# Kernel optimization log

Measured on AMD Instinct MI355X. Metric: run time of the kernel, lower is better.

## Reference

```python
import jax, jax.numpy as jnp
import numpy as np
import math

PI = math.pi

def setup_inputs() -> dict:
    key = jax.random.key(0)
    ks = jax.random.split(key, 12)
    B, L, D, K = 2, 2048, 256, 32
    s = 0.02
    return {
        "x":   jax.random.normal(ks[0], (B, L, D), dtype=jnp.float32),
        "kw1": jax.random.normal(ks[1], (D, D), dtype=jnp.float32) * s,
        "kb1": jnp.zeros((D,), dtype=jnp.float32),
        "kw2": jax.random.normal(ks[2], (K, D), dtype=jnp.float32) * s,
        "kb2": jnp.zeros((K,), dtype=jnp.float32),
        "qw1": jax.random.normal(ks[3], (D, D), dtype=jnp.float32) * s,
        "qb1": jnp.zeros((D,), dtype=jnp.float32),
        "qw2": jax.random.normal(ks[4], (K, D), dtype=jnp.float32) * s,
        "qb2": jnp.zeros((K,), dtype=jnp.float32),
        "vw":  jax.random.normal(ks[5], (D, D), dtype=jnp.float32) * s,
        "vb":  jnp.zeros((D,), dtype=jnp.float32),
    }

def _encode_phase(x, w1, b1, w2, b2):
    # Sequential(Linear, Tanh, Linear) followed by outer tanh * pi in forward
    h = jnp.tanh(jnp.einsum('bld,ed->ble', x, w1) + b1)
    return jnp.tanh(jnp.einsum('bld,kd->blk', h, w2) + b2) * PI

def reference(x, kw1, kb1, kw2, kb2, qw1, qb1, qw2, qb2, vw, vb):
    B, L, D = x.shape
    key_phase = _encode_phase(x, kw1, kb1, kw2, kb2)    # [B,L,K]
    query_phase = _encode_phase(x, qw1, qb1, qw2, qb2)  # [B,L,K]
    K = key_phase.shape[-1]
    value = jnp.einsum('bld,ed->ble', x, vw) + vb       # [B,L,D]

    cos_k = jnp.cos(key_phase)[..., None]               # [B,L,K,1]
    sin_k = jnp.sin(key_phase)[..., None]
    v_exp = value[:, :, None, :]                        # [B,L,1,D]
    mem_real = jnp.cumsum(cos_k * v_exp, axis=1)        # [B,L,K,D]
    mem_imag = jnp.cumsum(sin_k * v_exp, axis=1)

    cos_q = jnp.cos(query_phase)[..., None]
    sin_q = jnp.sin(query_phase)[..., None]
    retrieved = jnp.sum(mem_real * cos_q + mem_imag * sin_q, axis=2)  # [B,L,D]

    positions = jnp.arange(1, L + 1, dtype=x.dtype)
    norm = jnp.sqrt(positions * K)[None, :, None]
    return retrieved / norm
```

## Files before the change

kernel.cpp:

```cpp
#include <hip/hip_runtime.h>
#include <hip/hip_bf16.h>
#include <math.h>

typedef float v4f   __attribute__((ext_vector_type(4)));
typedef float f32x4 __attribute__((ext_vector_type(4)));
typedef short s16x8 __attribute__((ext_vector_type(8)));
typedef __hip_bfloat16 bf16;

#define PI_F 3.14159265358979323846f


__device__ inline unsigned short f2bf(float f) {
    unsigned int b = __float_as_uint(f);
    unsigned int r = (b + 0x7FFFu + ((b >> 16) & 1u)) >> 16;
    return (unsigned short)r;
}
__device__ inline float bf2f(unsigned short u) {
    return __uint_as_float(((unsigned int)u) << 16);
}
__device__ inline void cvt8(const float* __restrict__ src, unsigned short* dst) {
    v4f a = *(const v4f*)src, b = *(const v4f*)(src + 4);
    ushort4 u0, u1;
    u0.x = f2bf(a[0]); u0.y = f2bf(a[1]); u0.z = f2bf(a[2]); u0.w = f2bf(a[3]);
    u1.x = f2bf(b[0]); u1.y = f2bf(b[1]); u1.z = f2bf(b[2]); u1.w = f2bf(b[3]);
    *(ushort4*)dst = u0; *(ushort4*)(dst + 4) = u1;
}

__global__ __launch_bounds__(256) void k_cvtw(
    const float* __restrict__ kw1, const float* __restrict__ qw1,
    const float* __restrict__ vw,  const float* __restrict__ kw2,
    const float* __restrict__ qw2, bf16* __restrict__ Wb, bf16* __restrict__ W2b)
{
    int i8 = blockIdx.x * 256 + threadIdx.x;
    int r = i8 >> 5, c8 = (i8 & 31) * 8;
    const float* src;
    unsigned short* dst;
    if (r < 768) {
        src = (r < 256) ? kw1 + (size_t)r * 256
            : (r < 512) ? qw1 + (size_t)(r - 256) * 256
                        : vw  + (size_t)(r - 512) * 256;
        dst = (unsigned short*)Wb + (size_t)r * 256;
    } else {
        int r2 = r - 768;
        src = (r2 < 32) ? kw2 + (size_t)r2 * 256 : qw2 + (size_t)(r2 - 32) * 256;
        dst = (unsigned short*)W2b + (size_t)r2 * 256;
    }
    cvt8(src + c8, dst + c8);
}

__global__ __launch_bounds__(512) void k_fused(
    const float* __restrict__ X,   const bf16* __restrict__ Wb,
    const float* __restrict__ kb1, const float* __restrict__ qb1,
    const float* __restrict__ vb,  const bf16* __restrict__ W2b,
    const float* __restrict__ kb2, const float* __restrict__ qb2,
    float* __restrict__ KP, float* __restrict__ QP,
    bf16* __restrict__ Vb, bf16* __restrict__ SRg, bf16* __restrict__ SIg)
{
    __shared__ __align__(16) unsigned char smem[50688];
    unsigned short* Abf = (unsigned short*)smem;
    unsigned short* Hkq = (unsigned short*)(smem + 8448);
    unsigned short* Vt  = (unsigned short*)(smem + 25088);
    unsigned short* CKc = (unsigned short*)(smem + 45568);
    unsigned short* CKs = (unsigned short*)(smem + 48128);
    const int tid = threadIdx.x, bid = blockIdx.x;
    const int lane = tid & 63, wid = tid >> 6;
    const int lrow = lane & 15, lk8 = (lane >> 4) * 8, t0 = (lane >> 4) * 4;
    const int bb = bid >> 7, hc = bid & 127;
    const int row0 = bb * 2048 + hc * 16;

    {
        int r = tid >> 5, c8 = (tid & 31) * 8;
        cvt8(X + (size_t)(row0 + r) * 256 + c8, &Abf[r * 264 + c8]);
    }
    {
        s16x8 z = {};
        { int r = tid >> 1, h = tid & 1; *(s16x8*)&Vt[r * 40 + 16 + h * 8] = z; }
        if (tid < 64)       { int r = tid >> 1, h = tid & 1;
                              *(s16x8*)&CKc[r * 40 + 16 + h * 8] = z; }
        else if (tid < 128) { int r = (tid - 64) >> 1, h = tid & 1;
                              *(s16x8*)&CKs[r * 40 + 16 + h * 8] = z; }
    }
    __syncthreads();

    const int nb = wid * 96;
    const unsigned short* Wu = (const unsigned short*)Wb;
    f32x4 acc[6] = {};
    for (int k0 = 0; k0 < 256; k0 += 32) {
        s16x8 a = *(const s16x8*)&Abf[lrow * 264 + k0 + lk8];
        #pragma unroll
        for (int nf = 0; nf < 6; ++nf) {
            s16x8 b = *(const s16x8*)(Wu + (size_t)(nb + nf * 16 + lrow) * 256 + k0 + lk8);
            acc[nf] = __builtin_amdgcn_mfma_f32_16x16x32_bf16(a, b, acc[nf], 0, 0, 0);
        }
    }
    #pragma unroll
    for (int nf = 0; nf < 6; ++nf) {
        int n = nb + nf * 16 + lrow;
        float bias = (n < 256) ? kb1[n] : (n < 512) ? qb1[n - 256] : vb[n - 512];
        if (n < 512) {
            #pragma unroll
            for (int r = 0; r < 4; ++r)
                Hkq[(t0 + r) * 520 + n] = f2bf(tanhf(acc[nf][r] + bias));
        } else {
            int d = n - 512;
            ushort4 u;
            u.x = f2bf(acc[nf][0] + bias); u.y = f2bf(acc[nf][1] + bias);
            u.z = f2bf(acc[nf][2] + bias); u.w = f2bf(acc[nf][3] + bias);
            *(ushort4*)&Vt[d * 40 + t0] = u;
            unsigned short* Vg = (unsigned short*)Vb + (size_t)(row0 + t0) * 256 + d;
            Vg[0] = u.x; Vg[256] = u.y; Vg[512] = u.z; Vg[768] = u.w;
        }
    }
    __syncthreads();

    if (wid < 4) {
        const int which = wid >> 1, nf = wid & 1;
        const unsigned short* W2u = (const unsigned short*)W2b
            + (size_t)(which * 32 + nf * 16 + lrow) * 256;
        f32x4 u = {};
        for (int k0 = 0; k0 < 256; k0 += 32) {
            s16x8 a = *(const s16x8*)&Hkq[lrow * 520 + which * 256 + k0 + lk8];
            s16x8 b = *(const s16x8*)(W2u + k0 + lk8);
            u = __builtin_amdgcn_mfma_f32_16x16x32_bf16(a, b, u, 0, 0, 0);
        }
        const int outk = nf * 16 + lrow;
        const float bias = (which ? qb2 : kb2)[outk];
        float* dst = which ? QP : KP;
        float cs[4], sn[4];
        #pragma unroll
        for (int r = 0; r < 4; ++r) {
            float ph = tanhf(u[r] + bias) * PI_F;
            __sincosf(ph, &sn[r], &cs[r]);
            int row = row0 + t0 + r;
            dst[(size_t)row * 64 + outk]      = cs[r];
            dst[(size_t)row * 64 + 32 + outk] = sn[r];
        }
        if (which == 0) {
            ushort4 uc, us;
            uc.x = f2bf(cs[0]); uc.y = f2bf(cs[1]); uc.z = f2bf(cs[2]); uc.w = f2bf(cs[3]);
            us.x = f2bf(sn[0]); us.y = f2bf(sn[1]); us.z = f2bf(sn[2]); us.w = f2bf(sn[3]);
            *(ushort4*)&CKc[outk * 40 + t0] = uc;
            *(ushort4*)&CKs[outk * 40 + t0] = us;
        }
    }
    __syncthreads();

    {
        f32x4 zz = {};
        s16x8 ac0 = *(const s16x8*)&CKc[lrow * 40 + lk8];
        s16x8 ac1 = *(const s16x8*)&CKc[(16 + lrow) * 40 + lk8];
        s16x8 as0 = *(const s16x8*)&CKs[lrow * 40 + lk8];
        s16x8 as1 = *(const s16x8*)&CKs[(16 + lrow) * 40 + lk8];
        unsigned short* SRu = (unsigned short*)SRg;
        unsigned short* SIu = (unsigned short*)SIg;
        #pragma unroll
        for (int nf = 0; nf < 2; ++nf) {
            int dcol = wid * 32 + nf * 16 + lrow;
            s16x8 bv = *(const s16x8*)&Vt[dcol * 40 + lk8];
            f32x4 r0 = __builtin_amdgcn_mfma_f32_16x16x32_bf16(ac0, bv, zz, 0, 0, 0);
            f32x4 r1 = __builtin_amdgcn_mfma_f32_16x16x32_bf16(ac1, bv, zz, 0, 0, 0);
            f32x4 i0 = __builtin_amdgcn_mfma_f32_16x16x32_bf16(as0, bv, zz, 0, 0, 0);
            f32x4 i1 = __builtin_amdgcn_mfma_f32_16x16x32_bf16(as1, bv, zz, 0, 0, 0);
            size_t base = (((size_t)(bb * 128 + hc)) * 32) * 256 + dcol;
            #pragma unroll
            for (int r = 0; r < 4; ++r) {
                int ka = t0 + r, kb_ = 16 + t0 + r;
                SRu[base + (size_t)ka  * 256] = f2bf(r0[r]);
                SRu[base + (size_t)kb_ * 256] = f2bf(r1[r]);
                SIu[base + (size_t)ka  * 256] = f2bf(i0[r]);
                SIu[base + (size_t)kb_ * 256] = f2bf(i1[r]);
            }
        }
    }
}

__global__ __launch_bounds__(512) void k_scan(
    const bf16* __restrict__ SRh, const bf16* __restrict__ SIh,
    bf16* __restrict__ PFR, bf16* __restrict__ PFI)
{
    int gid = blockIdx.x * 512 + threadIdx.x;
    int e2 = gid & 4095, seg = (gid >> 12) & 7, ri = (gid >> 15) & 1, b = gid >> 16;
    const unsigned short* S = (const unsigned short*)(ri ? SIh : SRh);
    unsigned short* PF = (unsigned short*)(ri ? PFI : PFR);
    const size_t col = (size_t)e2 * 2;
    const size_t hbase = (size_t)(b * 128) * 8192 + col;
    float r0 = 0.f, r1 = 0.f;
    for (int hp = 0; hp < seg * 16; ++hp) {
        ushort2 u = *(const ushort2*)(S + hbase + (size_t)hp * 8192);
        r0 += bf2f(u.x); r1 += bf2f(u.y);
    }
    #pragma unroll
    for (int j = 0; j < 8; ++j) {
        int c = seg * 8 + j;
        ushort2 w; w.x = f2bf(r0); w.y = f2bf(r1);
        *(ushort2*)(PF + (size_t)(b * 64 + c) * 8192 + col) = w;
        ushort2 u0 = *(const ushort2*)(S + hbase + (size_t)(2 * c)     * 8192);
        ushort2 u1 = *(const ushort2*)(S + hbase + (size_t)(2 * c + 1) * 8192);
        r0 += bf2f(u0.x) + bf2f(u1.x);
        r1 += bf2f(u0.y) + bf2f(u1.y);
    }
}

__global__ __launch_bounds__(512) void k_attnout(
    const float* __restrict__ KP, const float* __restrict__ QP,
    const bf16* __restrict__ Vb,
    const bf16* __restrict__ PFR, const bf16* __restrict__ PFI,
    float* __restrict__ out)
{
    __shared__ float sm[18560];
    float* QPc = sm;
    float* KPc = sm + 2176;
    float* Sl  = sm + 4352;
    const int tid = threadIdx.x, bid = blockIdx.x;
    const int group = tid >> 8, t256 = tid & 255;
    float* grp  = sm + 5504 + group * 6528;
    float* vall = grp;
    float* PRl  = grp + 2176;
    float* PIl  = grp + 4352;
    const int b = bid >> 7, c = (bid >> 1) & 63, dhh = bid & 1;
    const int dh = dhh * 2 + group;
    const int row0 = b * 2048 + c * 32;

    #pragma unroll
    for (int it = 0; it < 2; ++it) {
        int idx = t256 + it * 256, t = idx >> 4, j4 = idx & 15;
        *(v4f*)&QPc[t * 68 + j4 * 4] = *(const v4f*)(QP + (size_t)(row0 + t) * 64 + j4 * 4);
        *(v4f*)&KPc[t * 68 + j4 * 4] = *(const v4f*)(KP + (size_t)(row0 + t) * 64 + j4 * 4);
    }
    {
        int t = t256 >> 3, e8 = (t256 & 7) * 8;
        s16x8 u = *(const s16x8*)((const unsigned short*)Vb
                                  + (size_t)(row0 + t) * 256 + dh * 64 + e8);
        #pragma unroll
        for (int j = 0; j < 8; ++j) vall[t * 68 + e8 + j] = bf2f((unsigned short)u[j]);
    }
    {
        int k = t256 >> 3, dg = t256 & 7;
        size_t pb = ((size_t)(b * 64 + c)) * 8192 + k * 256 + dh * 64 + dg * 8;
        s16x8 ur = *(const s16x8*)((const unsigned short*)PFR + pb);
        s16x8 ui = *(const s16x8*)((const unsigned short*)PFI + pb);
        #pragma unroll
        for (int j = 0; j < 8; ++j) {
            PRl[k * 68 + dg * 8 + j] = bf2f((unsigned short)ur[j]);
            PIl[k * 68 + dg * 8 + j] = bf2f((unsigned short)ui[j]);
        }
    }
    __syncthreads();
    {
        const int sl = t256 >> 3, tq = t256 & 7;
        float s4[4] = {0.f, 0.f, 0.f, 0.f};
        for (int j4 = 0; j4 < 16; ++j4) {
            v4f q4 = *(const v4f*)&QPc[sl * 68 + j4 * 4];
            #pragma unroll
            for (int i = 0; i < 4; ++i) {
                v4f k4 = *(const v4f*)&KPc[(tq * 4 + i) * 68 + j4 * 4];
                s4[i] += q4[0]*k4[0] + q4[1]*k4[1] + q4[2]*k4[2] + q4[3]*k4[3];
            }
        }
        #pragma unroll
        for (int i = 0; i < 4; ++i) {
            int t = tq * 4 + i;
            Sl[sl * 36 + t] = (t <= sl) ? s4[i] : 0.f;
        }
    }
    __syncthreads();
    const int l = t256 & 31, dq = t256 >> 5;
    const int d0 = dq * 8;
    float acc[8] = {};
    for (int k = 0; k < 32; ++k) {
        float qc = QPc[l * 68 + k], qs = QPc[l * 68 + 32 + k];
        #pragma unroll
        for (int j4 = 0; j4 < 2; ++j4) {
            v4f pr = *(const v4f*)&PRl[k * 68 + d0 + j4 * 4];
            v4f pi = *(const v4f*)&PIl[k * 68 + d0 + j4 * 4];
            #pragma unroll
            for (int x = 0; x < 4; ++x)
                acc[j4 * 4 + x] += qc * pr[x] + qs * pi[x];
        }
    }
    for (int t = 0; t < 32; ++t) {
        float s = Sl[l * 36 + t];
        #pragma unroll
        for (int j4 = 0; j4 < 2; ++j4) {
            v4f v4_ = *(const v4f*)&vall[t * 68 + d0 + j4 * 4];
            #pragma unroll
            for (int x = 0; x < 4; ++x)
                acc[j4 * 4 + x] = fmaf(s, v4_[x], acc[j4 * 4 + x]);
        }
    }
    const int gl = c * 32 + l;
    const float inv = rsqrtf((float)((gl + 1) * 32));
    const size_t ob = ((size_t)(b * 2048 + gl)) * 256 + dh * 64 + d0;
    #pragma unroll
    for (int j4 = 0; j4 < 2; ++j4) {
        v4f v;
        #pragma unroll
        for (int x = 0; x < 4; ++x) v[x] = acc[j4 * 4 + x] * inv;
        *(v4f*)(out + ob + j4 * 4) = v;
    }
}

extern "C" void kernel_launch(void* const* d_in, const int* in_sizes, int n_in,
                              void* d_out, int out_size, void* d_ws, size_t ws_size,
                              hipStream_t stream)
{
    const float* x   = (const float*)d_in[0];
    const float* kw1 = (const float*)d_in[1];
    const float* kb1 = (const float*)d_in[2];
    const float* kw2 = (const float*)d_in[3];
    const float* kb2 = (const float*)d_in[4];
    const float* qw1 = (const float*)d_in[5];
    const float* qb1 = (const float*)d_in[6];
    const float* qw2 = (const float*)d_in[7];
    const float* qb2 = (const float*)d_in[8];
    const float* vw  = (const float*)d_in[9];
    const float* vb  = (const float*)d_in[10];
    float* out = (float*)d_out;

    char* ws = (char*)d_ws;
    float* KP  = (float*)ws; ws += (size_t)4096 * 64 * 4;
    float* QP  = (float*)ws; ws += (size_t)4096 * 64 * 4;
    bf16*  Wb  = (bf16*)ws;  ws += (size_t)768 * 256 * 2;
    bf16*  W2b = (bf16*)ws;  ws += (size_t)64 * 256 * 2;
    bf16*  Vb  = (bf16*)ws;  ws += (size_t)4096 * 256 * 2;
    bf16*  SRh = (bf16*)ws;  ws += (size_t)2 * 128 * 32 * 256 * 2;
    bf16*  SIh = (bf16*)ws;  ws += (size_t)2 * 128 * 32 * 256 * 2;
    bf16*  PFR = (bf16*)ws;  ws += (size_t)2 * 64 * 32 * 256 * 2;
    bf16*  PFI = (bf16*)ws;  ws += (size_t)2 * 64 * 32 * 256 * 2;

    k_cvtw   <<<104, 256, 0, stream>>>(kw1, qw1, vw, kw2, qw2, Wb, W2b);
    k_fused  <<<256, 512, 0, stream>>>(x, Wb, kb1, qb1, vb, W2b, kb2, qb2,
                                       KP, QP, Vb, SRh, SIh);
    k_scan   <<<256, 512, 0, stream>>>(SRh, SIh, PFR, PFI);
    k_attnout<<<256, 512, 0, stream>>>(KP, QP, Vb, PFR, PFI, out);
}
```

Before: 62.43 us.

## Merge four kernels into one persistent kernel with software grid barriers

Replaces the weight-conversion, fused projection, scan and output kernels with a single 256-block kernel. The stages are separated by a hand-written grid barrier built on per-block flags and a release word in workspace, which is zeroed by a memset before each launch. This is meant to remove the launch gaps and tail effects between the four kernels. In exchange it adds barrier polling cost and a memset, and it depends on all 256 blocks being resident at once (512 threads, about 74 KB LDS each), or the barrier deadlocks.

```diff
diff --git a/kernel.cpp b/kernel.cpp
--- a/kernel.cpp
+++ b/kernel.cpp
@@ -26,277 +26,310 @@
     *(ushort4*)dst = u0; *(ushort4*)(dst + 4) = u1;
 }
 
-__global__ __launch_bounds__(256) void k_cvtw(
-    const float* __restrict__ kw1, const float* __restrict__ qw1,
-    const float* __restrict__ vw,  const float* __restrict__ kw2,
-    const float* __restrict__ qw2, bf16* __restrict__ Wb, bf16* __restrict__ W2b)
+__device__ inline void gridbar(int* flags, int* go, int epoch) {
+    __syncthreads();
+    const int tid = threadIdx.x, bid = blockIdx.x;
+    if (tid == 0) {
+        __threadfence();
+        __hip_atomic_store(&flags[bid], epoch, __ATOMIC_RELAXED,
+                           __HIP_MEMORY_SCOPE_AGENT);
+    }
+    if (bid == 0 && tid < 64) {
+        for (;;) {
+            int ok = 1;
+            #pragma unroll
+            for (int j = 0; j < 4; ++j)
+                ok &= (__hip_atomic_load(&flags[tid + 64 * j], __ATOMIC_RELAXED,
+                                         __HIP_MEMORY_SCOPE_AGENT) >= epoch);
+            if (__all(ok)) break;
+            __builtin_amdgcn_s_sleep(1);
+        }
+        if (tid == 0)
+            __hip_atomic_store(go, epoch, __ATOMIC_RELAXED,
+                               __HIP_MEMORY_SCOPE_AGENT);
+    }
+    if (tid == 0) {
+        while (__hip_atomic_load(go, __ATOMIC_RELAXED,
+                                 __HIP_MEMORY_SCOPE_AGENT) < epoch)
+            __builtin_amdgcn_s_sleep(2);
+        __threadfence();
+    }
+    __syncthreads();
+}
+
+__global__ __launch_bounds__(512) void k_mega(
+    const float* __restrict__ X,
+    const float* __restrict__ kw1, const float* __restrict__ kb1,
+    const float* __restrict__ kw2, const float* __restrict__ kb2,
+    const float* __restrict__ qw1, const float* __restrict__ qb1,
+    const float* __restrict__ qw2, const float* __restrict__ qb2,
+    const float* __restrict__ vw,  const float* __restrict__ vb,
+    float* __restrict__ KP, float* __restrict__ QP,
+    bf16* __restrict__ Wb, bf16* __restrict__ W2b, bf16* __restrict__ Vb,
+    bf16* __restrict__ SRg, bf16* __restrict__ SIg,
+    bf16* __restrict__ PFR, bf16* __restrict__ PFI,
+    float* __restrict__ out, int* __restrict__ bar)
 {
-    int i8 = blockIdx.x * 256 + threadIdx.x;
-    int r = i8 >> 5, c8 = (i8 & 31) * 8;
-    const float* src;
-    unsigned short* dst;
-    if (r < 768) {
-        src = (r < 256) ? kw1 + (size_t)r * 256
-            : (r < 512) ? qw1 + (size_t)(r - 256) * 256
-                        : vw  + (size_t)(r - 512) * 256;
-        dst = (unsigned short*)Wb + (size_t)r * 256;
-    } else {
-        int r2 = r - 768;
-        src = (r2 < 32) ? kw2 + (size_t)r2 * 256 : qw2 + (size_t)(r2 - 32) * 256;
-        dst = (unsigned short*)W2b + (size_t)r2 * 256;
-    }
-    cvt8(src + c8, dst + c8);
-}
-
-__global__ __launch_bounds__(512) void k_fused(
-    const float* __restrict__ X,   const bf16* __restrict__ Wb,
-    const float* __restrict__ kb1, const float* __restrict__ qb1,
-    const float* __restrict__ vb,  const bf16* __restrict__ W2b,
-    const float* __restrict__ kb2, const float* __restrict__ qb2,
-    float* __restrict__ KP, float* __restrict__ QP,
-    bf16* __restrict__ Vb, bf16* __restrict__ SRg, bf16* __restrict__ SIg)
-{
-    __shared__ __align__(16) unsigned char smem[50688];
-    unsigned short* Abf = (unsigned short*)smem;
-    unsigned short* Hkq = (unsigned short*)(smem + 8448);
-    unsigned short* Vt  = (unsigned short*)(smem + 25088);
-    unsigned short* CKc = (unsigned short*)(smem + 45568);
-    unsigned short* CKs = (unsigned short*)(smem + 48128);
+    __shared__ __align__(16) unsigned char smem[74240];
     const int tid = threadIdx.x, bid = blockIdx.x;
-    const int lane = tid & 63, wid = tid >> 6;
-    const int lrow = lane & 15, lk8 = (lane >> 4) * 8, t0 = (lane >> 4) * 4;
-    const int bb = bid >> 7, hc = bid & 127;
-    const int row0 = bb * 2048 + hc * 16;
+    int* flags = bar;
+    int* go    = bar + 320;
 
     {
-        int r = tid >> 5, c8 = (tid & 31) * 8;
-        cvt8(X + (size_t)(row0 + r) * 256 + c8, &Abf[r * 264 + c8]);
-    }
+        int gid = bid * 512 + tid;
+        if (gid < 26624) {
+            int r = gid >> 5, c8 = (gid & 31) * 8;
+            const float* src; unsigned short* dst;
+            if (r < 768) {
+                src = (r < 256) ? kw1 + (size_t)r * 256
+                    : (r < 512) ? qw1 + (size_t)(r - 256) * 256
+                                : vw  + (size_t)(r - 512) * 256;
+                dst = (unsigned short*)Wb + (size_t)r * 256;
+            } else {
+                int r2 = r - 768;
+                src = (r2 < 32) ? kw2 + (size_t)r2 * 256
+                                : qw2 + (size_t)(r2 - 32) * 256;
+                dst = (unsigned short*)W2b + (size_t)r2 * 256;
+            }
+            cvt8(src + c8, dst + c8);
+        }
+    }
+    gridbar(flags, go, 1);
+
     {
-        s16x8 z = {};
-        { int r = tid >> 1, h = tid & 1; *(s16x8*)&Vt[r * 40 + 16 + h * 8] = z; }
-        if (tid < 64)       { int r = tid >> 1, h = tid & 1;
-                              *(s16x8*)&CKc[r * 40 + 16 + h * 8] = z; }
-        else if (tid < 128) { int r = (tid - 64) >> 1, h = tid & 1;
-                              *(s16x8*)&CKs[r * 40 + 16 + h * 8] = z; }
-    }
-    __syncthreads();
-
-    const int nb = wid * 96;
-    const unsigned short* Wu = (const unsigned short*)Wb;
-    f32x4 acc[6] = {};
-    for (int k0 = 0; k0 < 256; k0 += 32) {
-        s16x8 a = *(const s16x8*)&Abf[lrow * 264 + k0 + lk8];
+        unsigned short* Abf = (unsigned short*)smem;
+        unsigned short* Hkq = (unsigned short*)(smem + 8448);
+        unsigned short* Vt  = (unsigned short*)(smem + 25088);
+        unsigned short* CKc = (unsigned short*)(smem + 45568);
+        unsigned short* CKs = (unsigned short*)(smem + 48128);
+        const int lane = tid & 63, wid = tid >> 6;
+        const int lrow = lane & 15, lk8 = (lane >> 4) * 8, t0 = (lane >> 4) * 4;
+        const int bb = bid >> 7, hc = bid & 127;
+        const int row0 = bb * 2048 + hc * 16;
+
+        {
+            int r = tid >> 5, c8 = (tid & 31) * 8;
+            cvt8(X + (size_t)(row0 + r) * 256 + c8, &Abf[r * 264 + c8]);
+        }
+        {
+            s16x8 z = {};
+            { int r = tid >> 1, h = tid & 1; *(s16x8*)&Vt[r * 40 + 16 + h * 8] = z; }
+            if (tid < 64)       { int r = tid >> 1, h = tid & 1;
+                                  *(s16x8*)&CKc[r * 40 + 16 + h * 8] = z; }
+            else if (tid < 128) { int r = (tid - 64) >> 1, h = tid & 1;
+                                  *(s16x8*)&CKs[r * 40 + 16 + h * 8] = z; }
+        }
+        __syncthreads();
+
+        const int nb = wid * 96;
+        const unsigned short* Wu = (const unsigned short*)Wb;
+        f32x4 acc[6] = {};
+        for (int k0 = 0; k0 < 256; k0 += 32) {
+            s16x8 a = *(const s16x8*)&Abf[lrow * 264 + k0 + lk8];
+            #pragma unroll
+            for (int nf = 0; nf < 6; ++nf) {
+                s16x8 b = *(const s16x8*)(Wu + (size_t)(nb + nf * 16 + lrow) * 256 + k0 + lk8);
+                acc[nf] = __builtin_amdgcn_mfma_f32_16x16x32_bf16(a, b, acc[nf], 0, 0, 0);
+            }
+        }
         #pragma unroll
         for (int nf = 0; nf < 6; ++nf) {
-            s16x8 b = *(const s16x8*)(Wu + (size_t)(nb + nf * 16 + lrow) * 256 + k0 + lk8);
-            acc[nf] = __builtin_amdgcn_mfma_f32_16x16x32_bf16(a, b, acc[nf], 0, 0, 0);
-        }
-    }
-    #pragma unroll
-    for (int nf = 0; nf < 6; ++nf) {
-        int n = nb + nf * 16 + lrow;
-        float bias = (n < 256) ? kb1[n] : (n < 512) ? qb1[n - 256] : vb[n - 512];
-        if (n < 512) {
-            #pragma unroll
-            for (int r = 0; r < 4; ++r)
-                Hkq[(t0 + r) * 520 + n] = f2bf(tanhf(acc[nf][r] + bias));
-        } else {
-            int d = n - 512;
-            ushort4 u;
-            u.x = f2bf(acc[nf][0] + bias); u.y = f2bf(acc[nf][1] + bias);
-            u.z = f2bf(acc[nf][2] + bias); u.w = f2bf(acc[nf][3] + bias);
-            *(ushort4*)&Vt[d * 40 + t0] = u;
-            unsigned short* Vg = (unsigned short*)Vb + (size_t)(row0 + t0) * 256 + d;
-            Vg[0] = u.x; Vg[256] = u.y; Vg[512] = u.z; Vg[768] = u.w;
-        }
-    }
-    __syncthreads();
-
-    if (wid < 4) {
-        const int which = wid >> 1, nf = wid & 1;
-        const unsigned short* W2u = (const unsigned short*)W2b
-            + (size_t)(which * 32 + nf * 16 + lrow) * 256;
-        f32x4 u = {};
-        for (int k0 = 0; k0 < 256; k0 += 32) {
-            s16x8 a = *(const s16x8*)&Hkq[lrow * 520 + which * 256 + k0 + lk8];
-            s16x8 b = *(const s16x8*)(W2u + k0 + lk8);
-            u = __builtin_amdgcn_mfma_f32_16x16x32_bf16(a, b, u, 0, 0, 0);
-        }
-        const int outk = nf * 16 + lrow;
-        const float bias = (which ? qb2 : kb2)[outk];
-        float* dst = which ? QP : KP;
-        float cs[4], sn[4];
-        #pragma unroll
-        for (int r = 0; r < 4; ++r) {
-            float ph = tanhf(u[r] + bias) * PI_F;
-            __sincosf(ph, &sn[r], &cs[r]);
-            int row = row0 + t0 + r;
-            dst[(size_t)row * 64 + outk]      = cs[r];
-            dst[(size_t)row * 64 + 32 + outk] = sn[r];
-        }
-        if (which == 0) {
-            ushort4 uc, us;
-            uc.x = f2bf(cs[0]); uc.y = f2bf(cs[1]); uc.z = f2bf(cs[2]); uc.w = f2bf(cs[3]);
-            us.x = f2bf(sn[0]); us.y = f2bf(sn[1]); us.z = f2bf(sn[2]); us.w = f2bf(sn[3]);
-            *(ushort4*)&CKc[outk * 40 + t0] = uc;
-            *(ushort4*)&CKs[outk * 40 + t0] = us;
-        }
-    }
-    __syncthreads();
+            int n = nb + nf * 16 + lrow;
+            float bias = (n < 256) ? kb1[n] : (n < 512) ? qb1[n - 256] : vb[n - 512];
+            if (n < 512) {
+                #pragma unroll
+                for (int r = 0; r < 4; ++r)
+                    Hkq[(t0 + r) * 520 + n] = f2bf(tanhf(acc[nf][r] + bias));
+            } else {
+                int d = n - 512;
+                ushort4 u;
+                u.x = f2bf(acc[nf][0] + bias); u.y = f2bf(acc[nf][1] + bias);
+                u.z = f2bf(acc[nf][2] + bias); u.w = f2bf(acc[nf][3] + bias);
+                *(ushort4*)&Vt[d * 40 + t0] = u;
+                unsigned short* Vg = (unsigned short*)Vb + (size_t)(row0 + t0) * 256 + d;
+                Vg[0] = u.x; Vg[256] = u.y; Vg[512] = u.z; Vg[768] = u.w;
+            }
+        }
+        __syncthreads();
+
+        if (wid < 4) {
+            const int which = wid >> 1, nf = wid & 1;
+            const unsigned short* W2u = (const unsigned short*)W2b
+                + (size_t)(which * 32 + nf * 16 + lrow) * 256;
+            f32x4 u = {};
+            for (int k0 = 0; k0 < 256; k0 += 32) {
+                s16x8 a = *(const s16x8*)&Hkq[lrow * 520 + which * 256 + k0 + lk8];
+                s16x8 b = *(const s16x8*)(W2u + k0 + lk8);
+                u = __builtin_amdgcn_mfma_f32_16x16x32_bf16(a, b, u, 0, 0, 0);
+            }
+            const int outk = nf * 16 + lrow;
+            const float bias = (which ? qb2 : kb2)[outk];
+            float* dst = which ? QP : KP;
+            float cs[4], sn[4];
+            #pragma unroll
+            for (int r = 0; r < 4; ++r) {
+                float ph = tanhf(u[r] + bias) * PI_F;
+                __sincosf(ph, &sn[r], &cs[r]);
+                int row = row0 + t0 + r;
+                dst[(size_t)row * 64 + outk]      = cs[r];
+                dst[(size_t)row * 64 + 32 + outk] = sn[r];
+            }
+            if (which == 0) {
+                ushort4 uc, us;
+                uc.x = f2bf(cs[0]); uc.y = f2bf(cs[1]); uc.z = f2bf(cs[2]); uc.w = f2bf(cs[3]);
+                us.x = f2bf(sn[0]); us.y = f2bf(sn[1]); us.z = f2bf(sn[2]); us.w = f2bf(sn[3]);
+                *(ushort4*)&CKc[outk * 40 + t0] = uc;
+                *(ushort4*)&CKs[outk * 40 + t0] = us;
+            }
+        }
+        __syncthreads();
+
+        {
+            f32x4 zz = {};
+            s16x8 ac0 = *(const s16x8*)&CKc[lrow * 40 + lk8];
+            s16x8 ac1 = *(const s16x8*)&CKc[(16 + lrow) * 40 + lk8];
+            s16x8 as0 = *(const s16x8*)&CKs[lrow * 40 + lk8];
+            s16x8 as1 = *(const s16x8*)&CKs[(16 + lrow) * 40 + lk8];
+            unsigned short* SRu = (unsigned short*)SRg;
+            unsigned short* SIu = (unsigned short*)SIg;
+            #pragma unroll
+            for (int nf = 0; nf < 2; ++nf) {
+                int dcol = wid * 32 + nf * 16 + lrow;
+                s16x8 bv = *(const s16x8*)&Vt[dcol * 40 + lk8];
+                f32x4 r0 = __builtin_amdgcn_mfma_f32_16x16x32_bf16(ac0, bv, zz, 0, 0, 0);
+                f32x4 r1 = __builtin_amdgcn_mfma_f32_16x16x32_bf16(ac1, bv, zz, 0, 0, 0);
+                f32x4 i0 = __builtin_amdgcn_mfma_f32_16x16x32_bf16(as0, bv, zz, 0, 0, 0);
+                f32x4 i1 = __builtin_amdgcn_mfma_f32_16x16x32_bf16(as1, bv, zz, 0, 0, 0);
+                size_t base = (((size_t)(bb * 128 + hc)) * 32) * 256 + dcol;
+                #pragma unroll
+                for (int r = 0; r < 4; ++r) {
+                    int ka = t0 + r, kb_ = 16 + t0 + r;
+                    SRu[base + (size_t)ka  * 256] = f2bf(r0[r]);
+                    SRu[base + (size_t)kb_ * 256] = f2bf(r1[r]);
+                    SIu[base + (size_t)ka  * 256] = f2bf(i0[r]);
+                    SIu[base + (size_t)kb_ * 256] = f2bf(i1[r]);
+                }
+            }
+        }
+    }
+    gridbar(flags, go, 2);
 
     {
-        f32x4 zz = {};
-        s16x8 ac0 = *(const s16x8*)&CKc[lrow * 40 + lk8];
-        s16x8 ac1 = *(const s16x8*)&CKc[(16 + lrow) * 40 + lk8];
-        s16x8 as0 = *(const s16x8*)&CKs[lrow * 40 + lk8];
-        s16x8 as1 = *(const s16x8*)&CKs[(16 + lrow) * 40 + lk8];
-        unsigned short* SRu = (unsigned short*)SRg;
-        unsigned short* SIu = (unsigned short*)SIg;
-        #pragma unroll
-        for (int nf = 0; nf < 2; ++nf) {
-            int dcol = wid * 32 + nf * 16 + lrow;
-            s16x8 bv = *(const s16x8*)&Vt[dcol * 40 + lk8];
-            f32x4 r0 = __builtin_amdgcn_mfma_f32_16x16x32_bf16(ac0, bv, zz, 0, 0, 0);
-            f32x4 r1 = __builtin_amdgcn_mfma_f32_16x16x32_bf16(ac1, bv, zz, 0, 0, 0);
-            f32x4 i0 = __builtin_amdgcn_mfma_f32_16x16x32_bf16(as0, bv, zz, 0, 0, 0);
-            f32x4 i1 = __builtin_amdgcn_mfma_f32_16x16x32_bf16(as1, bv, zz, 0, 0, 0);
-            size_t base = (((size_t)(bb * 128 + hc)) * 32) * 256 + dcol;
-            #pragma unroll
-            for (int r = 0; r < 4; ++r) {
-                int ka = t0 + r, kb_ = 16 + t0 + r;
-                SRu[base + (size_t)ka  * 256] = f2bf(r0[r]);
-                SRu[base + (size_t)kb_ * 256] = f2bf(r1[r]);
-                SIu[base + (size_t)ka  * 256] = f2bf(i0[r]);
-                SIu[base + (size_t)kb_ * 256] = f2bf(i1[r]);
-            }
-        }
-    }
-}
-
-__global__ __launch_bounds__(512) void k_scan(
-    const bf16* __restrict__ SRh, const bf16* __restrict__ SIh,
-    bf16* __restrict__ PFR, bf16* __restrict__ PFI)
-{
-    int gid = blockIdx.x * 512 + threadIdx.x;
-    int e2 = gid & 4095, seg = (gid >> 12) & 7, ri = (gid >> 15) & 1, b = gid >> 16;
-    const unsigned short* S = (const unsigned short*)(ri ? SIh : SRh);
-    unsigned short* PF = (unsigned short*)(ri ? PFI : PFR);
-    const size_t col = (size_t)e2 * 2;
-    const size_t hbase = (size_t)(b * 128) * 8192 + col;
-    float r0 = 0.f, r1 = 0.f;
-    for (int hp = 0; hp < seg * 16; ++hp) {
-        ushort2 u = *(const ushort2*)(S + hbase + (size_t)hp * 8192);
-        r0 += bf2f(u.x); r1 += bf2f(u.y);
-    }
-    #pragma unroll
-    for (int j = 0; j < 8; ++j) {
-        int c = seg * 8 + j;
-        ushort2 w; w.x = f2bf(r0); w.y = f2bf(r1);
-        *(ushort2*)(PF + (size_t)(b * 64 + c) * 8192 + col) = w;
-        ushort2 u0 = *(const ushort2*)(S + hbase + (size_t)(2 * c)     * 8192);
-        ushort2 u1 = *(const ushort2*)(S + hbase + (size_t)(2 * c + 1) * 8192);
-        r0 += bf2f(u0.x) + bf2f(u1.x);
-        r1 += bf2f(u0.y) + bf2f(u1.y);
-    }
-}
-
-__global__ __launch_bounds__(512) void k_attnout(
-    const float* __restrict__ KP, const float* __restrict__ QP,
-    const bf16* __restrict__ Vb,
-    const bf16* __restrict__ PFR, const bf16* __restrict__ PFI,
-    float* __restrict__ out)
-{
-    __shared__ float sm[18560];
-    float* QPc = sm;
-    float* KPc = sm + 2176;
-    float* Sl  = sm + 4352;
-    const int tid = threadIdx.x, bid = blockIdx.x;
-    const int group = tid >> 8, t256 = tid & 255;
-    float* grp  = sm + 5504 + group * 6528;
-    float* vall = grp;
-    float* PRl  = grp + 2176;
-    float* PIl  = grp + 4352;
-    const int b = bid >> 7, c = (bid >> 1) & 63, dhh = bid & 1;
-    const int dh = dhh * 2 + group;
-    const int row0 = b * 2048 + c * 32;
-
-    #pragma unroll
-    for (int it = 0; it < 2; ++it) {
-        int idx = t256 + it * 256, t = idx >> 4, j4 = idx & 15;
-        *(v4f*)&QPc[t * 68 + j4 * 4] = *(const v4f*)(QP + (size_t)(row0 + t) * 64 + j4 * 4);
-        *(v4f*)&KPc[t * 68 + j4 * 4] = *(const v4f*)(KP + (size_t)(row0 + t) * 64 + j4 * 4);
-    }
-    {
-        int t = t256 >> 3, e8 = (t256 & 7) * 8;
-        s16x8 u = *(const s16x8*)((const unsigned short*)Vb
-                                  + (size_t)(row0 + t) * 256 + dh * 64 + e8);
-        #pragma unroll
-        for (int j = 0; j < 8; ++j) vall[t * 68 + e8 + j] = bf2f((unsigned short)u[j]);
-    }
-    {
-        int k = t256 >> 3, dg = t256 & 7;
-        size_t pb = ((size_t)(b * 64 + c)) * 8192 + k * 256 + dh * 64 + dg * 8;
-        s16x8 ur = *(const s16x8*)((const unsigned short*)PFR + pb);
-        s16x8 ui = *(const s16x8*)((const unsigned short*)PFI + pb);
+        int gid = bid * 512 + tid;
+        int e2 = gid & 4095, seg = (gid >> 12) & 7, ri = (gid >> 15) & 1, b = gid >> 16;
+        const unsigned short* S = (const unsigned short*)(ri ? SIg : SRg);
+        unsigned short* PF = (unsigned short*)(ri ? PFI : PFR);
+        const size_t col = (size_t)e2 * 2;
+        const size_t hbase = (size_t)(b * 128) * 8192 + col;
+        float r0 = 0.f, r1 = 0.f;
+        for (int hp = 0; hp < seg * 16; ++hp) {
+            ushort2 u = *(const ushort2*)(S + hbase + (size_t)hp * 8192);
+            r0 += bf2f(u.x); r1 += bf2f(u.y);
+        }
         #pragma unroll
         for (int j = 0; j < 8; ++j) {
-            PRl[k * 68 + dg * 8 + j] = bf2f((unsigned short)ur[j]);
-            PIl[k * 68 + dg * 8 + j] = bf2f((unsigned short)ui[j]);
-        }
-    }
-    __syncthreads();
+            int c = seg * 8 + j;
+            ushort2 w; w.x = f2bf(r0); w.y = f2bf(r1);
+            *(ushort2*)(PF + (size_t)(b * 64 + c) * 8192 + col) = w;
+            ushort2 u0 = *(const ushort2*)(S + hbase + (size_t)(2 * c)     * 8192);
+            ushort2 u1 = *(const ushort2*)(S + hbase + (size_t)(2 * c + 1) * 8192);
+            r0 += bf2f(u0.x) + bf2f(u1.x);
+            r1 += bf2f(u0.y) + bf2f(u1.y);
+        }
+    }
+    gridbar(flags, go, 3);
+
     {
-        const int sl = t256 >> 3, tq = t256 & 7;
-        float s4[4] = {0.f, 0.f, 0.f, 0.f};
-        for (int j4 = 0; j4 < 16; ++j4) {
-            v4f q4 = *(const v4f*)&QPc[sl * 68 + j4 * 4];
+        float* sm  = (float*)smem;
+        float* QPc = sm;
+        float* KPc = sm + 2176;
+        float* Sl  = sm + 4352;
+        const int group = tid >> 8, t256 = tid & 255;
+        float* grp  = sm + 5504 + group * 6528;
+        float* vall = grp;
+        float* PRl  = grp + 2176;
+        float* PIl  = grp + 4352;
+        const int b = bid >> 7, c = (bid >> 1) & 63, dhh = bid & 1;
+        const int dh = dhh * 2 + group;
+        const int row0 = b * 2048 + c * 32;
+
+        #pragma unroll
+        for (int it = 0; it < 2; ++it) {
+            int idx = t256 + it * 256, t = idx >> 4, j4 = idx & 15;
+            *(v4f*)&QPc[t * 68 + j4 * 4] = *(const v4f*)(QP + (size_t)(row0 + t) * 64 + j4 * 4);
+            *(v4f*)&KPc[t * 68 + j4 * 4] = *(const v4f*)(KP + (size_t)(row0 + t) * 64 + j4 * 4);
+        }
+        {
+            int t = t256 >> 3, e8 = (t256 & 7) * 8;
+            s16x8 u = *(const s16x8*)((const unsigned short*)Vb
+                                      + (size_t)(row0 + t) * 256 + dh * 64 + e8);
+            #pragma unroll
+            for (int j = 0; j < 8; ++j) vall[t * 68 + e8 + j] = bf2f((unsigned short)u[j]);
+        }
+        {
+            int k = t256 >> 3, dg = t256 & 7;
+            size_t pb = ((size_t)(b * 64 + c)) * 8192 + k * 256 + dh * 64 + dg * 8;
+            s16x8 ur = *(const s16x8*)((const unsigned short*)PFR + pb);
+            s16x8 ui = *(const s16x8*)((const unsigned short*)PFI + pb);
+            #pragma unroll
+            for (int j = 0; j < 8; ++j) {
+                PRl[k * 68 + dg * 8 + j] = bf2f((unsigned short)ur[j]);
+                PIl[k * 68 + dg * 8 + j] = bf2f((unsigned short)ui[j]);
+            }
+        }
+        __syncthreads();
+        {
+            const int sl = t256 >> 3, tq = t256 & 7;
+            float s4[4] = {0.f, 0.f, 0.f, 0.f};
+            for (int j4 = 0; j4 < 16; ++j4) {
+                v4f q4 = *(const v4f*)&QPc[sl * 68 + j4 * 4];
+                #pragma unroll
+                for (int i = 0; i < 4; ++i) {
+                    v4f k4 = *(const v4f*)&KPc[(tq * 4 + i) * 68 + j4 * 4];
+                    s4[i] += q4[0]*k4[0] + q4[1]*k4[1] + q4[2]*k4[2] + q4[3]*k4[3];
+                }
+            }
             #pragma unroll
             for (int i = 0; i < 4; ++i) {
-                v4f k4 = *(const v4f*)&KPc[(tq * 4 + i) * 68 + j4 * 4];
-                s4[i] += q4[0]*k4[0] + q4[1]*k4[1] + q4[2]*k4[2] + q4[3]*k4[3];
-            }
-        }
-        #pragma unroll
-        for (int i = 0; i < 4; ++i) {
-            int t = tq * 4 + i;
-            Sl[sl * 36 + t] = (t <= sl) ? s4[i] : 0.f;
-        }
-    }
-    __syncthreads();
-    const int l = t256 & 31, dq = t256 >> 5;
-    const int d0 = dq * 8;
-    float acc[8] = {};
-    for (int k = 0; k < 32; ++k) {
-        float qc = QPc[l * 68 + k], qs = QPc[l * 68 + 32 + k];
+                int t = tq * 4 + i;
+                Sl[sl * 36 + t] = (t <= sl) ? s4[i] : 0.f;
+            }
+        }
+        __syncthreads();
+        const int l = t256 & 31, dq = t256 >> 5;
+        const int d0 = dq * 8;
+        float acc[8] = {};
+        for (int k = 0; k < 32; ++k) {
+            float qc = QPc[l * 68 + k], qs = QPc[l * 68 + 32 + k];
+            #pragma unroll
+            for (int j4 = 0; j4 < 2; ++j4) {
+                v4f pr = *(const v4f*)&PRl[k * 68 + d0 + j4 * 4];
+                v4f pi = *(const v4f*)&PIl[k * 68 + d0 + j4 * 4];
+                #pragma unroll
+                for (int x = 0; x < 4; ++x)
+                    acc[j4 * 4 + x] += qc * pr[x] + qs * pi[x];
+            }
+        }
+        for (int t = 0; t < 32; ++t) {
+            float s = Sl[l * 36 + t];
+            #pragma unroll
+            for (int j4 = 0; j4 < 2; ++j4) {
+                v4f v4_ = *(const v4f*)&vall[t * 68 + d0 + j4 * 4];
+                #pragma unroll
+                for (int x = 0; x < 4; ++x)
+                    acc[j4 * 4 + x] = fmaf(s, v4_[x], acc[j4 * 4 + x]);
+            }
+        }
+        const int gl = c * 32 + l;
+        const float inv = rsqrtf((float)((gl + 1) * 32));
+        const size_t ob = ((size_t)(b * 2048 + gl)) * 256 + dh * 64 + d0;
         #pragma unroll
         for (int j4 = 0; j4 < 2; ++j4) {
-            v4f pr = *(const v4f*)&PRl[k * 68 + d0 + j4 * 4];
-            v4f pi = *(const v4f*)&PIl[k * 68 + d0 + j4 * 4];
-            #pragma unroll
-            for (int x = 0; x < 4; ++x)
-                acc[j4 * 4 + x] += qc * pr[x] + qs * pi[x];
-        }
-    }
-    for (int t = 0; t < 32; ++t) {
-        float s = Sl[l * 36 + t];
-        #pragma unroll
-        for (int j4 = 0; j4 < 2; ++j4) {
-            v4f v4_ = *(const v4f*)&vall[t * 68 + d0 + j4 * 4];
-            #pragma unroll
-            for (int x = 0; x < 4; ++x)
-                acc[j4 * 4 + x] = fmaf(s, v4_[x], acc[j4 * 4 + x]);
-        }
-    }
-    const int gl = c * 32 + l;
-    const float inv = rsqrtf((float)((gl + 1) * 32));
-    const size_t ob = ((size_t)(b * 2048 + gl)) * 256 + dh * 64 + d0;
-    #pragma unroll
-    for (int j4 = 0; j4 < 2; ++j4) {
-        v4f v;
-        #pragma unroll
-        for (int x = 0; x < 4; ++x) v[x] = acc[j4 * 4 + x] * inv;
-        *(v4f*)(out + ob + j4 * 4) = v;
+            v4f v;
+            #pragma unroll
+            for (int x = 0; x < 4; ++x) v[x] = acc[j4 * 4 + x] * inv;
+            *(v4f*)(out + ob + j4 * 4) = v;
+        }
     }
 }
 
@@ -318,6 +351,7 @@
     float* out = (float*)d_out;
 
     char* ws = (char*)d_ws;
+    int*   bar = (int*)ws;   ws += 2048;
     float* KP  = (float*)ws; ws += (size_t)4096 * 64 * 4;
     float* QP  = (float*)ws; ws += (size_t)4096 * 64 * 4;
     bf16*  Wb  = (bf16*)ws;  ws += (size_t)768 * 256 * 2;
@@ -328,9 +362,8 @@
     bf16*  PFR = (bf16*)ws;  ws += (size_t)2 * 64 * 32 * 256 * 2;
     bf16*  PFI = (bf16*)ws;  ws += (size_t)2 * 64 * 32 * 256 * 2;
 
-    k_cvtw   <<<104, 256, 0, stream>>>(kw1, qw1, vw, kw2, qw2, Wb, W2b);
-    k_fused  <<<256, 512, 0, stream>>>(x, Wb, kb1, qb1, vb, W2b, kb2, qb2,
-                                       KP, QP, Vb, SRh, SIh);
-    k_scan   <<<256, 512, 0, stream>>>(SRh, SIh, PFR, PFI);
-    k_attnout<<<256, 512, 0, stream>>>(KP, QP, Vb, PFR, PFI, out);
-}
+    hipMemsetAsync(bar, 0, 2048, stream);
+    k_mega<<<256, 512, 0, stream>>>(x, kw1, kb1, kw2, kb2, qw1, qb1, qw2, qb2,
+                                    vw, vb, KP, QP, Wb, W2b, Vb,
+                                    SRh, SIh, PFR, PFI, out, bar);
+}
```

New measurement: 100.8 us. +61.4%, slower.

## Fuse chunk prefix scan into attention output kernel, drop separate scan pass

Applied to the files above, without the earlier changes.

Removes the separate k_scan kernel and its PFR/PFI intermediate buffers. Each output block now sums its own prefix over the per-half-chunk partial states directly from SRh/SIh. The output kernel is split into 8 slices of 32 columns with 256 threads, which gives more blocks. This saves a launch and a global round trip, but early-to-late chunks do uneven work (up to 126 strided loads per thread), and the prefix reads are repeated across blocks.

```diff
diff --git a/kernel.cpp b/kernel.cpp
--- a/kernel.cpp
+++ b/kernel.cpp
@@ -48,7 +48,7 @@
     cvt8(src + c8, dst + c8);
 }
 
-__global__ __launch_bounds__(512) void k_fused(
+__global__ __launch_bounds__(512) void k_fusedH(
     const float* __restrict__ X,   const bf16* __restrict__ Wb,
     const float* __restrict__ kb1, const float* __restrict__ qb1,
     const float* __restrict__ vb,  const bf16* __restrict__ W2b,
@@ -161,7 +161,7 @@
             f32x4 r1 = __builtin_amdgcn_mfma_f32_16x16x32_bf16(ac1, bv, zz, 0, 0, 0);
             f32x4 i0 = __builtin_amdgcn_mfma_f32_16x16x32_bf16(as0, bv, zz, 0, 0, 0);
             f32x4 i1 = __builtin_amdgcn_mfma_f32_16x16x32_bf16(as1, bv, zz, 0, 0, 0);
-            size_t base = (((size_t)(bb * 128 + hc)) * 32) * 256 + dcol;
+            size_t base = (((size_t)bid) * 32) * 256 + dcol;
             #pragma unroll
             for (int r = 0; r < 4; ++r) {
                 int ka = t0 + r, kb_ = 16 + t0 + r;
@@ -174,80 +174,59 @@
     }
 }
 
-__global__ __launch_bounds__(512) void k_scan(
-    const bf16* __restrict__ SRh, const bf16* __restrict__ SIh,
-    bf16* __restrict__ PFR, bf16* __restrict__ PFI)
-{
-    int gid = blockIdx.x * 512 + threadIdx.x;
-    int e2 = gid & 4095, seg = (gid >> 12) & 7, ri = (gid >> 15) & 1, b = gid >> 16;
-    const unsigned short* S = (const unsigned short*)(ri ? SIh : SRh);
-    unsigned short* PF = (unsigned short*)(ri ? PFI : PFR);
-    const size_t col = (size_t)e2 * 2;
-    const size_t hbase = (size_t)(b * 128) * 8192 + col;
-    float r0 = 0.f, r1 = 0.f;
-    for (int hp = 0; hp < seg * 16; ++hp) {
-        ushort2 u = *(const ushort2*)(S + hbase + (size_t)hp * 8192);
-        r0 += bf2f(u.x); r1 += bf2f(u.y);
-    }
-    #pragma unroll
-    for (int j = 0; j < 8; ++j) {
-        int c = seg * 8 + j;
-        ushort2 w; w.x = f2bf(r0); w.y = f2bf(r1);
-        *(ushort2*)(PF + (size_t)(b * 64 + c) * 8192 + col) = w;
-        ushort2 u0 = *(const ushort2*)(S + hbase + (size_t)(2 * c)     * 8192);
-        ushort2 u1 = *(const ushort2*)(S + hbase + (size_t)(2 * c + 1) * 8192);
-        r0 += bf2f(u0.x) + bf2f(u1.x);
-        r1 += bf2f(u0.y) + bf2f(u1.y);
-    }
-}
-
-__global__ __launch_bounds__(512) void k_attnout(
+__global__ __launch_bounds__(256) void k_attnout(
     const float* __restrict__ KP, const float* __restrict__ QP,
     const bf16* __restrict__ Vb,
-    const bf16* __restrict__ PFR, const bf16* __restrict__ PFI,
+    const bf16* __restrict__ SRg, const bf16* __restrict__ SIg,
     float* __restrict__ out)
 {
-    __shared__ float sm[18560];
-    float* QPc = sm;
-    float* KPc = sm + 2176;
-    float* Sl  = sm + 4352;
-    const int tid = threadIdx.x, bid = blockIdx.x;
-    const int group = tid >> 8, t256 = tid & 255;
-    float* grp  = sm + 5504 + group * 6528;
-    float* vall = grp;
-    float* PRl  = grp + 2176;
-    float* PIl  = grp + 4352;
-    const int b = bid >> 7, c = (bid >> 1) & 63, dhh = bid & 1;
-    const int dh = dhh * 2 + group;
+    __shared__ float QPc[32 * 68], KPc[32 * 68], Sl[32 * 36];
+    __shared__ float vall[32 * 36], PRl[32 * 36], PIl[32 * 36];
+    const int tid = threadIdx.x;
+    const int b = blockIdx.x >> 6, c = blockIdx.x & 63;
+    const int dh = blockIdx.y;
     const int row0 = b * 2048 + c * 32;
 
     #pragma unroll
     for (int it = 0; it < 2; ++it) {
-        int idx = t256 + it * 256, t = idx >> 4, j4 = idx & 15;
+        int idx = tid + it * 256, t = idx >> 4, j4 = idx & 15;
         *(v4f*)&QPc[t * 68 + j4 * 4] = *(const v4f*)(QP + (size_t)(row0 + t) * 64 + j4 * 4);
         *(v4f*)&KPc[t * 68 + j4 * 4] = *(const v4f*)(KP + (size_t)(row0 + t) * 64 + j4 * 4);
     }
     {
-        int t = t256 >> 3, e8 = (t256 & 7) * 8;
-        s16x8 u = *(const s16x8*)((const unsigned short*)Vb
-                                  + (size_t)(row0 + t) * 256 + dh * 64 + e8);
-        #pragma unroll
-        for (int j = 0; j < 8; ++j) vall[t * 68 + e8 + j] = bf2f((unsigned short)u[j]);
-    }
-    {
-        int k = t256 >> 3, dg = t256 & 7;
-        size_t pb = ((size_t)(b * 64 + c)) * 8192 + k * 256 + dh * 64 + dg * 8;
-        s16x8 ur = *(const s16x8*)((const unsigned short*)PFR + pb);
-        s16x8 ui = *(const s16x8*)((const unsigned short*)PFI + pb);
-        #pragma unroll
-        for (int j = 0; j < 8; ++j) {
-            PRl[k * 68 + dg * 8 + j] = bf2f((unsigned short)ur[j]);
-            PIl[k * 68 + dg * 8 + j] = bf2f((unsigned short)ui[j]);
-        }
-    }
-    __syncthreads();
-    {
-        const int sl = t256 >> 3, tq = t256 & 7;
+        int t = tid >> 3, e4 = (tid & 7) * 4;
+        ushort4 u = *(const ushort4*)((const unsigned short*)Vb
+                                      + (size_t)(row0 + t) * 256 + dh * 32 + e4);
+        vall[t * 36 + e4 + 0] = bf2f(u.x);
+        vall[t * 36 + e4 + 1] = bf2f(u.y);
+        vall[t * 36 + e4 + 2] = bf2f(u.z);
+        vall[t * 36 + e4 + 3] = bf2f(u.w);
+    }
+    {
+        int k = tid >> 3, dg = tid & 7;
+        float pr[4] = {}, pi[4] = {};
+        const unsigned short* SRu = (const unsigned short*)SRg;
+        const unsigned short* SIu = (const unsigned short*)SIg;
+        size_t sb = ((size_t)(b * 128) * 32 + k) * 256 + dh * 32 + dg * 4;
+        const int hend = 2 * c;
+        #pragma unroll 4
+        for (int hp = 0; hp < hend; ++hp) {
+            ushort4 ur = *(const ushort4*)(SRu + sb + (size_t)hp * 8192);
+            ushort4 ui = *(const ushort4*)(SIu + sb + (size_t)hp * 8192);
+            pr[0] += bf2f(ur.x); pr[1] += bf2f(ur.y);
+            pr[2] += bf2f(ur.z); pr[3] += bf2f(ur.w);
+            pi[0] += bf2f(ui.x); pi[1] += bf2f(ui.y);
+            pi[2] += bf2f(ui.z); pi[3] += bf2f(ui.w);
+        }
+        #pragma unroll
+        for (int j = 0; j < 4; ++j) {
+            PRl[k * 36 + dg * 4 + j] = pr[j];
+            PIl[k * 36 + dg * 4 + j] = pi[j];
+        }
+    }
+    __syncthreads();
+    {
+        const int sl = tid >> 3, tq = tid & 7;
         float s4[4] = {0.f, 0.f, 0.f, 0.f};
         for (int j4 = 0; j4 < 16; ++j4) {
             v4f q4 = *(const v4f*)&QPc[sl * 68 + j4 * 4];
@@ -264,40 +243,31 @@
         }
     }
     __syncthreads();
-    const int l = t256 & 31, dq = t256 >> 5;
-    const int d0 = dq * 8;
-    float acc[8] = {};
+    const int l = tid & 31, dq = tid >> 5;
+    const int d0 = dq * 4;
+    float acc[4] = {};
     for (int k = 0; k < 32; ++k) {
         float qc = QPc[l * 68 + k], qs = QPc[l * 68 + 32 + k];
-        #pragma unroll
-        for (int j4 = 0; j4 < 2; ++j4) {
-            v4f pr = *(const v4f*)&PRl[k * 68 + d0 + j4 * 4];
-            v4f pi = *(const v4f*)&PIl[k * 68 + d0 + j4 * 4];
-            #pragma unroll
-            for (int x = 0; x < 4; ++x)
-                acc[j4 * 4 + x] += qc * pr[x] + qs * pi[x];
-        }
+        v4f pr = *(const v4f*)&PRl[k * 36 + d0];
+        v4f pi = *(const v4f*)&PIl[k * 36 + d0];
+        #pragma unroll
+        for (int x = 0; x < 4; ++x)
+            acc[x] += qc * pr[x] + qs * pi[x];
     }
     for (int t = 0; t < 32; ++t) {
         float s = Sl[l * 36 + t];
-        #pragma unroll
-        for (int j4 = 0; j4 < 2; ++j4) {
-            v4f v4_ = *(const v4f*)&vall[t * 68 + d0 + j4 * 4];
-            #pragma unroll
-            for (int x = 0; x < 4; ++x)
-                acc[j4 * 4 + x] = fmaf(s, v4_[x], acc[j4 * 4 + x]);
-        }
+        v4f v4_ = *(const v4f*)&vall[t * 36 + d0];
+        #pragma unroll
+        for (int x = 0; x < 4; ++x)
+            acc[x] = fmaf(s, v4_[x], acc[x]);
     }
     const int gl = c * 32 + l;
     const float inv = rsqrtf((float)((gl + 1) * 32));
-    const size_t ob = ((size_t)(b * 2048 + gl)) * 256 + dh * 64 + d0;
+    const size_t ob = ((size_t)(b * 2048 + gl)) * 256 + dh * 32 + d0;
+    v4f v;
     #pragma unroll
-    for (int j4 = 0; j4 < 2; ++j4) {
-        v4f v;
-        #pragma unroll
-        for (int x = 0; x < 4; ++x) v[x] = acc[j4 * 4 + x] * inv;
-        *(v4f*)(out + ob + j4 * 4) = v;
-    }
+    for (int x = 0; x < 4; ++x) v[x] = acc[x] * inv;
+    *(v4f*)(out + ob) = v;
 }
 
 extern "C" void kernel_launch(void* const* d_in, const int* in_sizes, int n_in,
@@ -325,12 +295,9 @@
     bf16*  Vb  = (bf16*)ws;  ws += (size_t)4096 * 256 * 2;
     bf16*  SRh = (bf16*)ws;  ws += (size_t)2 * 128 * 32 * 256 * 2;
     bf16*  SIh = (bf16*)ws;  ws += (size_t)2 * 128 * 32 * 256 * 2;
-    bf16*  PFR = (bf16*)ws;  ws += (size_t)2 * 64 * 32 * 256 * 2;
-    bf16*  PFI = (bf16*)ws;  ws += (size_t)2 * 64 * 32 * 256 * 2;
-
-    k_cvtw   <<<104, 256, 0, stream>>>(kw1, qw1, vw, kw2, qw2, Wb, W2b);
-    k_fused  <<<256, 512, 0, stream>>>(x, Wb, kb1, qb1, vb, W2b, kb2, qb2,
-                                       KP, QP, Vb, SRh, SIh);
-    k_scan   <<<256, 512, 0, stream>>>(SRh, SIh, PFR, PFI);
-    k_attnout<<<256, 512, 0, stream>>>(KP, QP, Vb, PFR, PFI, out);
-}
+
+    k_cvtw   <<<104,          256, 0, stream>>>(kw1, qw1, vw, kw2, qw2, Wb, W2b);
+    k_fusedH <<<256,          512, 0, stream>>>(x, Wb, kb1, qb1, vb, W2b, kb2, qb2,
+                                                KP, QP, Vb, SRh, SIh);
+    k_attnout<<<dim3(128, 8), 256, 0, stream>>>(KP, QP, Vb, SRh, SIh, out);
+}
```

Measured after the change: 72.38 us. 15.9% more time.
